# Optimization experiments

Measured on AMD Instinct MI355X. Metric: run time of the kernel, lower is better.

## Reference

```python
import jax, jax.numpy as jnp
import numpy as np

N_NODES = 50000
N_EDGES = 1600000
N_FEAT = 50
HID = 20
OUT_DIM = 10
N_GRAPHS = 64


def _glorot(key, shape):
    fan_in, fan_out = shape[0], shape[1]
    lim = float(np.sqrt(6.0 / (fan_in + fan_out)))
    return jax.random.uniform(key, shape, jnp.float32, -lim, lim)


def setup_inputs() -> dict:
    key = jax.random.key(0)
    ks = jax.random.split(key, 16)
    x = jax.random.normal(ks[0], (N_NODES, N_FEAT), jnp.float32)
    edge_index = jax.random.randint(ks[1], (2, N_EDGES), 0, N_NODES, jnp.int32)
    batch = jnp.sort(jax.random.randint(ks[2], (N_NODES,), 0, N_GRAPHS, jnp.int32))
    inp = {"x": x, "edge_index": edge_index, "batch": batch}
    # GraphConv layer params: lin_rel (weight+bias, applied to aggregated msgs), lin_root (no bias)
    dims = [(N_FEAT, HID), (HID, HID), (HID, HID)]
    for i, (di, do) in enumerate(dims, start=1):
        inp[f"W_rel{i}"] = _glorot(ks[3 * i], (di, do))
        inp[f"W_root{i}"] = _glorot(ks[3 * i + 1], (di, do))
        inp[f"b{i}"] = jnp.zeros((do,), jnp.float32)
    # final Linear on cat([max_pool, mean_pool]) -> in_features = 2*HID
    inp["W_lin"] = _glorot(ks[13], (2 * HID, OUT_DIM))
    inp["b_lin"] = jnp.zeros((OUT_DIM,), jnp.float32)
    return inp


def _graph_conv(x, src, dst, W_rel, W_root, b):
    # PyG GraphConv: aggregate raw neighbor features (sum), then linear.
    agg = jax.ops.segment_sum(x[src], dst, num_segments=N_NODES)  # [N, d_in]
    return agg @ W_rel + x @ W_root + b


def reference(x, edge_index, batch,
              W_rel1, W_root1, b1,
              W_rel2, W_root2, b2,
              W_rel3, W_root3, b3,
              W_lin, b_lin):
    src, dst = edge_index[0], edge_index[1]
    h = jax.nn.relu(_graph_conv(x, src, dst, W_rel1, W_root1, b1))
    h = jax.nn.relu(_graph_conv(h, src, dst, W_rel2, W_root2, b2))
    h = jax.nn.relu(_graph_conv(h, src, dst, W_rel3, W_root3, b3))
    # global max / mean pool per graph
    maxP = jax.ops.segment_max(h, batch, num_segments=N_GRAPHS)  # [G, HID]
    sums = jax.ops.segment_sum(h, batch, num_segments=N_GRAPHS)
    cnt = jax.ops.segment_sum(jnp.ones((h.shape[0], 1), h.dtype), batch, num_segments=N_GRAPHS)
    meanP = sums / jnp.maximum(cnt, 1.0)
    return jnp.concatenate([maxP, meanP], axis=-1) @ W_lin + b_lin
```

## Files before the change

### kernel.cpp

```cpp
#include <hip/hip_runtime.h>

#define N_NODES  50000
#define N_EDGES  1600000
#define N_FEAT   50
#define HID      20
#define OUT_DIM  10
#define N_GRAPHS 64

#define NBUCK 196
#define BCAP  10240
#define EPB   (N_EDGES/256)


__global__ __launch_bounds__(1024) void init_all(int* __restrict__ gcur,
        float* __restrict__ gmax, float* __restrict__ gsum, float* __restrict__ gcnt) {
    int t = threadIdx.x;
    if (t < NBUCK) gcur[t] = t * BCAP;
    for (int i = t; i < N_GRAPHS * HID; i += 1024) { gmax[i] = 0.f; gsum[i] = 0.f; }
    if (t < N_GRAPHS) gcnt[t] = 0.f;
}


__global__ __launch_bounds__(256) void gemm50(const float* __restrict__ x,
        const float* __restrict__ Wrel, const float* __restrict__ Wroot,
        const float* __restrict__ b,
        float* __restrict__ y, float* __restrict__ acc) {
    __shared__ float sWrel[N_FEAT * HID];
    __shared__ float sWroot[N_FEAT * HID];
    for (int i = threadIdx.x; i < N_FEAT * HID; i += 256) {
        sWrel[i]  = Wrel[i];
        sWroot[i] = Wroot[i];
    }
    __syncthreads();
    int idx = blockIdx.x * 256 + threadIdx.x;
    if (idx >= N_NODES * HID) return;
    int n = idx / HID, j = idx % HID;
    const float* xr = x + n * N_FEAT;
    float a0 = 0.0f, a1 = b[j];
    #pragma unroll
    for (int k = 0; k < N_FEAT; ++k) {
        float xv = xr[k];
        a0 = fmaf(xv, sWrel[k * HID + j], a0);
        a1 = fmaf(xv, sWroot[k * HID + j], a1);
    }
    y[idx]   = a0;
    acc[idx] = a1;
}


__global__ __launch_bounds__(1024) void bucket_scatter(const int* __restrict__ dst,
        const int* __restrict__ src, int* __restrict__ gcur,
        unsigned int* __restrict__ padded) {
    __shared__ unsigned int ep[EPB];
    __shared__ unsigned int ep2[EPB];
    __shared__ int cnt[256];
    __shared__ int scn[256];
    __shared__ int lofs[256];
    __shared__ int gbase[256];
    __shared__ int lcur[256];
    int t = threadIdx.x;
    if (t < 256) cnt[t] = 0;
    __syncthreads();
    int e0 = blockIdx.x * EPB;
    for (int i = t; i < EPB; i += 1024) {
        int d = dst[e0 + i];
        int s = src[e0 + i];
        ep[i] = ((unsigned int)d << 16) | (unsigned int)s;
        atomicAdd(&cnt[d >> 8], 1);
    }
    __syncthreads();
    if (t < 256) scn[t] = cnt[t];
    __syncthreads();
    for (int d = 1; d < 256; d <<= 1) {
        int u = 0;
        if (t < 256 && t >= d) u = scn[t - d];
        __syncthreads();
        if (t < 256) scn[t] += u;
        __syncthreads();
    }
    if (t < NBUCK) {
        int excl = scn[t] - cnt[t];
        lofs[t] = excl;
        lcur[t] = excl;
        gbase[t] = atomicAdd(&gcur[t], cnt[t]);
    }
    __syncthreads();
    for (int i = t; i < EPB; i += 1024) {
        unsigned int e = ep[i];
        int p = atomicAdd(&lcur[e >> 24], 1);
        ep2[p] = e;
    }
    __syncthreads();
    for (int i = t; i < EPB; i += 1024) {
        unsigned int e = ep2[i];
        int b = e >> 24;
        int gp = gbase[b] + (i - lofs[b]);
        if (gp < (b + 1) * BCAP) padded[gp] = e;
    }
}


__global__ __launch_bounds__(1024) void bucket_build(const int* __restrict__ gcur,
        const unsigned int* __restrict__ padded, unsigned short* __restrict__ csr16,
        int* __restrict__ start, int* __restrict__ endp) {
    __shared__ unsigned short eo[BCAP];
    __shared__ int cnt4[4][256];
    __shared__ int cur4[4][256];
    __shared__ int scn[256];
    int g = blockIdx.x, t = threadIdx.x;
    int wg = t >> 8;
    int base = g * BCAP;
    int m = min(gcur[g] - base, BCAP);
    if (t < 256) { cnt4[0][t] = 0; cnt4[1][t] = 0; cnt4[2][t] = 0; cnt4[3][t] = 0; }
    __syncthreads();
    for (int i = t; i < m; i += 1024)
        atomicAdd(&cnt4[wg][(padded[base + i] >> 16) & 255u], 1);
    __syncthreads();
    int c0 = 0, c1 = 0, c2 = 0, c3 = 0, tot = 0;
    if (t < 256) {
        c0 = cnt4[0][t]; c1 = cnt4[1][t]; c2 = cnt4[2][t]; c3 = cnt4[3][t];
        tot = c0 + c1 + c2 + c3;
        scn[t] = tot;
    }
    __syncthreads();
    for (int d = 1; d < 256; d <<= 1) {
        int u = 0;
        if (t < 256 && t >= d) u = scn[t - d];
        __syncthreads();
        if (t < 256) scn[t] += u;
        __syncthreads();
    }
    if (t < 256) {
        int excl = scn[t] - tot;
        cur4[0][t] = excl;
        cur4[1][t] = excl + c0;
        cur4[2][t] = excl + c0 + c1;
        cur4[3][t] = excl + c0 + c1 + c2;
        int node = g * 256 + t;
        if (node < N_NODES) {
            start[node] = base + excl;
            endp[node]  = base + excl + tot;
        }
    }
    __syncthreads();
    for (int i = t; i < m; i += 1024) {
        unsigned int e = padded[base + i];
        int p = atomicAdd(&cur4[wg][(e >> 16) & 255u], 1);
        eo[p] = (unsigned short)(e & 0xFFFFu);
    }
    __syncthreads();
    for (int i = t; i < m; i += 1024) csr16[base + i] = eo[i];
}


__global__ __launch_bounds__(320) void gather_gemm(const int* __restrict__ offs,
        const int* __restrict__ cend, const unsigned short* __restrict__ csr,
        const float* __restrict__ y_in, const float* __restrict__ accp,
        const float* __restrict__ Wrel, const float* __restrict__ Wroot,
        const float* __restrict__ b,
        float* __restrict__ y_out, float* __restrict__ acc_out) {
    __shared__ float sWrel[HID * HID];
    __shared__ float sWroot[HID * HID];
    __shared__ float sb[HID];
    __shared__ float rh[64][HID];
    for (int i = threadIdx.x; i < HID * HID; i += 320) {
        sWrel[i]  = Wrel[i];
        sWroot[i] = Wroot[i];
    }
    if (threadIdx.x < HID) sb[threadIdx.x] = b[threadIdx.x];
    int local = threadIdx.x / 5;
    int q     = threadIdx.x % 5;
    int node  = blockIdx.x * 64 + local;
    bool valid = node < N_NODES;
    if (valid) {
        int a = offs[node], e = cend[node];
        float4 s0 = make_float4(0.f, 0.f, 0.f, 0.f);
        float4 s1 = make_float4(0.f, 0.f, 0.f, 0.f);
        int k = a;
        for (; k + 3 < e; k += 4) {
            int sn0 = csr[k], sn1 = csr[k + 1], sn2 = csr[k + 2], sn3 = csr[k + 3];
            float4 v0 = *(const float4*)(y_in + sn0 * HID + q * 4);
            float4 v1 = *(const float4*)(y_in + sn1 * HID + q * 4);
            float4 v2 = *(const float4*)(y_in + sn2 * HID + q * 4);
            float4 v3 = *(const float4*)(y_in + sn3 * HID + q * 4);
            s0.x += v0.x + v2.x; s0.y += v0.y + v2.y;
            s0.z += v0.z + v2.z; s0.w += v0.w + v2.w;
            s1.x += v1.x + v3.x; s1.y += v1.y + v3.y;
            s1.z += v1.z + v3.z; s1.w += v1.w + v3.w;
        }
        for (; k < e; ++k) {
            int sn = csr[k];
            float4 v = *(const float4*)(y_in + sn * HID + q * 4);
            s0.x += v.x; s0.y += v.y; s0.z += v.z; s0.w += v.w;
        }
        float4 av = *((const float4*)(accp + node * HID) + q);
        rh[local][q * 4 + 0] = fmaxf(av.x + s0.x + s1.x, 0.f);
        rh[local][q * 4 + 1] = fmaxf(av.y + s0.y + s1.y, 0.f);
        rh[local][q * 4 + 2] = fmaxf(av.z + s0.z + s1.z, 0.f);
        rh[local][q * 4 + 3] = fmaxf(av.w + s0.w + s1.w, 0.f);
    }
    __syncthreads();
    if (!valid) return;
    int j0 = q * 4;
    float y0 = 0.f, y1 = 0.f, y2 = 0.f, y3 = 0.f;
    float a0 = sb[j0], a1 = sb[j0 + 1], a2 = sb[j0 + 2], a3 = sb[j0 + 3];
    #pragma unroll
    for (int k = 0; k < HID; ++k) {
        float hv = rh[local][k];
        const float* wr = sWrel  + k * HID + j0;
        const float* wo = sWroot + k * HID + j0;
        y0 = fmaf(hv, wr[0], y0); y1 = fmaf(hv, wr[1], y1);
        y2 = fmaf(hv, wr[2], y2); y3 = fmaf(hv, wr[3], y3);
        a0 = fmaf(hv, wo[0], a0); a1 = fmaf(hv, wo[1], a1);
        a2 = fmaf(hv, wo[2], a2); a3 = fmaf(hv, wo[3], a3);
    }
    *((float4*)(y_out   + node * HID) + q) = make_float4(y0, y1, y2, y3);
    *((float4*)(acc_out + node * HID) + q) = make_float4(a0, a1, a2, a3);
}


__global__ __launch_bounds__(320) void gather_pool(const int* __restrict__ offs,
        const int* __restrict__ cend, const unsigned short* __restrict__ csr,
        const float* __restrict__ y, const float* __restrict__ accp,
        const int* __restrict__ batch,
        float* __restrict__ gmax, float* __restrict__ gsum, float* __restrict__ gcnt) {
    __shared__ float bufA[64 * HID];
    __shared__ float bufB[64 * HID];
    __shared__ int   lcnt[64];
    int t = threadIdx.x;
    int local = t / 5;
    int q     = t % 5;
    int n0    = blockIdx.x * 64;
    int node  = n0 + local;
    int nvalid = min(64, N_NODES - n0);
    int nlast  = n0 + nvalid - 1;
    int g0   = batch[n0];
    int span = batch[nlast] - g0 + 1;
    bool valid = node < N_NODES;

    float v0 = 0.f, v1 = 0.f, v2 = 0.f, v3 = 0.f;
    if (valid) {
        int a = offs[node], e = cend[node];
        float4 s0 = make_float4(0.f, 0.f, 0.f, 0.f);
        float4 s1 = make_float4(0.f, 0.f, 0.f, 0.f);
        int k = a;
        for (; k + 3 < e; k += 4) {
            int sn0 = csr[k], sn1 = csr[k + 1], sn2 = csr[k + 2], sn3 = csr[k + 3];
            float4 w0 = *(const float4*)(y + sn0 * HID + q * 4);
            float4 w1 = *(const float4*)(y + sn1 * HID + q * 4);
            float4 w2 = *(const float4*)(y + sn2 * HID + q * 4);
            float4 w3 = *(const float4*)(y + sn3 * HID + q * 4);
            s0.x += w0.x + w2.x; s0.y += w0.y + w2.y;
            s0.z += w0.z + w2.z; s0.w += w0.w + w2.w;
            s1.x += w1.x + w3.x; s1.y += w1.y + w3.y;
            s1.z += w1.z + w3.z; s1.w += w1.w + w3.w;
        }
        for (; k < e; ++k) {
            int sn = csr[k];
            float4 w = *(const float4*)(y + sn * HID + q * 4);
            s0.x += w.x; s0.y += w.y; s0.z += w.z; s0.w += w.w;
        }
        float4 av = *((const float4*)(accp + node * HID) + q);
        v0 = fmaxf(av.x + s0.x + s1.x, 0.f);
        v1 = fmaxf(av.y + s0.y + s1.y, 0.f);
        v2 = fmaxf(av.z + s0.z + s1.z, 0.f);
        v3 = fmaxf(av.w + s0.w + s1.w, 0.f);
    }

    if (span == 1) {
        int j0 = q * 4;
        bufA[local * HID + j0 + 0] = v0;
        bufA[local * HID + j0 + 1] = v1;
        bufA[local * HID + j0 + 2] = v2;
        bufA[local * HID + j0 + 3] = v3;
        __syncthreads();
        int j = t % HID, r = t / HID;
        float m = 0.f, s = 0.f;
        #pragma unroll
        for (int rr = 0; rr < 4; ++rr) {
            float hv = bufA[(r + rr * 16) * HID + j];
            m = fmaxf(m, hv);
            s += hv;
        }
        bufB[r * HID + j] = m;
        bufB[320 + r * HID + j] = s;
        __syncthreads();
        if (t < HID) {
            float mm = 0.f, ss = 0.f;
            #pragma unroll
            for (int rr = 0; rr < 16; ++rr) {
                mm = fmaxf(mm, bufB[rr * HID + t]);
                ss += bufB[320 + rr * HID + t];
            }
            atomicMax((int*)&gmax[g0 * HID + t], __float_as_int(mm));
            atomicAdd(&gsum[g0 * HID + t], ss);
        }
        if (t == 0) atomicAdd(&gcnt[g0], (float)nvalid);
    } else {
        for (int i = t; i < 64 * HID; i += 320) { bufA[i] = 0.f; bufB[i] = 0.f; }
        if (t < 64) lcnt[t] = 0;
        __syncthreads();
        if (valid) {
            int li = batch[node] - g0;
            int j0 = q * 4;
            atomicMax((int*)&bufA[li * HID + j0 + 0], __float_as_int(v0));
            atomicMax((int*)&bufA[li * HID + j0 + 1], __float_as_int(v1));
            atomicMax((int*)&bufA[li * HID + j0 + 2], __float_as_int(v2));
            atomicMax((int*)&bufA[li * HID + j0 + 3], __float_as_int(v3));
            atomicAdd(&bufB[li * HID + j0 + 0], v0);
            atomicAdd(&bufB[li * HID + j0 + 1], v1);
            atomicAdd(&bufB[li * HID + j0 + 2], v2);
            atomicAdd(&bufB[li * HID + j0 + 3], v3);
            if (q == 0) atomicAdd(&lcnt[li], 1);
        }
        __syncthreads();
        for (int i = t; i < span * HID; i += 320) {
            int li = i / HID, j = i % HID;
            atomicMax((int*)&gmax[(g0 + li) * HID + j], __float_as_int(bufA[i]));
            atomicAdd(&gsum[(g0 + li) * HID + j], bufB[i]);
        }
        if (t < span) atomicAdd(&gcnt[g0 + t], (float)lcnt[t]);
    }
}


__global__ __launch_bounds__(640) void final_lin(const float* __restrict__ gmax,
        const float* __restrict__ gsum, const float* __restrict__ gcnt,
        const float* __restrict__ Wlin, const float* __restrict__ blin,
        float* __restrict__ out) {
    __shared__ float sW[2 * HID * OUT_DIM];
    for (int i = threadIdx.x; i < 2 * HID * OUT_DIM; i += 640) sW[i] = Wlin[i];
    __syncthreads();
    int idx = threadIdx.x;
    if (idx >= N_GRAPHS * OUT_DIM) return;
    int g = idx / OUT_DIM, o = idx % OUT_DIM;
    float c = fmaxf(gcnt[g], 1.0f);
    float a = blin[o];
    #pragma unroll
    for (int j = 0; j < HID; ++j) {
        a = fmaf(gmax[g * HID + j], sW[j * OUT_DIM + o], a);
        a = fmaf(gsum[g * HID + j] / c, sW[(HID + j) * OUT_DIM + o], a);
    }
    out[idx] = a;
}

extern "C" void kernel_launch(void* const* d_in, const int* in_sizes, int n_in,
                              void* d_out, int out_size, void* d_ws, size_t ws_size,
                              hipStream_t stream) {
    const float* x      = (const float*)d_in[0];
    const int*   ei     = (const int*)  d_in[1];
    const int*   batch  = (const int*)  d_in[2];
    const float* Wrel1  = (const float*)d_in[3];
    const float* Wroot1 = (const float*)d_in[4];
    const float* b1     = (const float*)d_in[5];
    const float* Wrel2  = (const float*)d_in[6];
    const float* Wroot2 = (const float*)d_in[7];
    const float* b2     = (const float*)d_in[8];
    const float* Wrel3  = (const float*)d_in[9];
    const float* Wroot3 = (const float*)d_in[10];
    const float* b3     = (const float*)d_in[11];
    const float* Wlin   = (const float*)d_in[12];
    const float* blin   = (const float*)d_in[13];
    float* out = (float*)d_out;

    char* ws = (char*)d_ws;
    const size_t NB   = (size_t)N_NODES * HID * sizeof(float);
    const size_t PB   = (size_t)NBUCK * BCAP * sizeof(int);
    const size_t CB   = (size_t)NBUCK * BCAP * sizeof(unsigned short);
    float*          yA     = (float*)(ws);
    float*          yB     = (float*)(ws + NB);
    float*          accA   = (float*)(ws + 2 * NB);
    float*          accB   = (float*)(ws + 3 * NB);
    unsigned int*   padded = (unsigned int*)(ws + 4 * NB);
    unsigned short* csr16  = (unsigned short*)(ws + 4 * NB + PB);
    int*            start  = (int*)(ws + 4 * NB + PB + CB);
    int*            endp   = start + N_NODES;
    int*            gcur   = endp + N_NODES;
    float*          gmax   = (float*)(gcur + NBUCK + 4);
    float*          gsum   = gmax + N_GRAPHS * HID;
    float*          gcnt   = gsum + N_GRAPHS * HID;

    const int* src = ei;
    const int* dst = ei + N_EDGES;

    const int gN = (N_NODES * HID + 255) / 256;
    const int gG = (N_NODES + 63) / 64;

    init_all<<<1, 1024, 0, stream>>>(gcur, gmax, gsum, gcnt);
    bucket_scatter<<<256, 1024, 0, stream>>>(dst, src, gcur, padded);
    bucket_build<<<NBUCK, 1024, 0, stream>>>(gcur, padded, csr16, start, endp);

    gemm50<<<gN, 256, 0, stream>>>(x, Wrel1, Wroot1, b1, yA, accA);
    gather_gemm<<<gG, 320, 0, stream>>>(start, endp, csr16, yA, accA,
                                        Wrel2, Wroot2, b2, yB, accB);
    gather_gemm<<<gG, 320, 0, stream>>>(start, endp, csr16, yB, accB,
                                        Wrel3, Wroot3, b3, yA, accA);
    gather_pool<<<gG, 320, 0, stream>>>(start, endp, csr16, yA, accA, batch,
                                        gmax, gsum, gcnt);
    final_lin<<<1, 640, 0, stream>>>(gmax, gsum, gcnt, Wlin, blin, out);
}
```

Before: 124.2 us.

## Fuse graph-build and GEMM kernels, sort nodes by degree for balanced gathers

Merges the first GEMM and the edge bucket scatter into one launch using disjoint block ranges, and replaces init_all with a memset. Fuses CSR bucket build with the layer-2 gather+GEMM so the block reuses its shared-memory edge list. Gathers now run in 256-node blocks that pair heavy and light nodes via a per-bucket degree-sorted permutation. Pooling uses segment ranges instead of atomics. This cuts launch count and load imbalance but lowers the number of blocks per gather kernel (196) and adds an O(256^2) rank sort per block.

```diff
diff --git a/kernel.cpp b/kernel.cpp
--- a/kernel.cpp
+++ b/kernel.cpp
@@ -10,66 +10,120 @@
 #define NBUCK 196
 #define BCAP  10240
 #define EPB   (N_EDGES/256)
-
-
-__global__ __launch_bounds__(1024) void init_all(int* __restrict__ gcur,
+#define G50B  977
+
+
+__global__ __launch_bounds__(1024) void k1_gemm_scatter(
+        const float* __restrict__ x, const float* __restrict__ Wrel,
+        const float* __restrict__ Wroot, const float* __restrict__ b,
+        float* __restrict__ y, float* __restrict__ acc,
+        const int* __restrict__ dst, const int* __restrict__ srcv,
+        int* __restrict__ gcur, unsigned int* __restrict__ padded,
         float* __restrict__ gmax, float* __restrict__ gsum, float* __restrict__ gcnt) {
+    __shared__ char smem[55120];
     int t = threadIdx.x;
-    if (t < NBUCK) gcur[t] = t * BCAP;
-    for (int i = t; i < N_GRAPHS * HID; i += 1024) { gmax[i] = 0.f; gsum[i] = 0.f; }
-    if (t < N_GRAPHS) gcnt[t] = 0.f;
-}
-
-
-__global__ __launch_bounds__(256) void gemm50(const float* __restrict__ x,
+    if (blockIdx.x < G50B) {
+        if (blockIdx.x == 0) {
+            for (int i = t; i < N_GRAPHS * HID; i += 1024) { gmax[i] = 0.f; gsum[i] = 0.f; }
+            if (t < N_GRAPHS) gcnt[t] = 0.f;
+        }
+        float* sWrel  = (float*)smem;
+        float* sWroot = sWrel + N_FEAT * HID;
+        for (int i = t; i < N_FEAT * HID; i += 1024) { sWrel[i] = Wrel[i]; sWroot[i] = Wroot[i]; }
+        __syncthreads();
+        int idx = blockIdx.x * 1024 + t;
+        if (idx < N_NODES * HID) {
+            int n = idx / HID, j = idx % HID;
+            const float* xr = x + n * N_FEAT;
+            float a0 = 0.f, a1 = b[j];
+            #pragma unroll
+            for (int k = 0; k < N_FEAT; ++k) {
+                float xv = xr[k];
+                a0 = fmaf(xv, sWrel[k * HID + j], a0);
+                a1 = fmaf(xv, sWroot[k * HID + j], a1);
+            }
+            y[idx] = a0; acc[idx] = a1;
+        }
+    } else {
+        unsigned int* ep   = (unsigned int*)smem;
+        unsigned int* ep2  = ep + EPB;
+        int* cnt   = (int*)(ep2 + EPB);
+        int* scn   = cnt + 256;
+        int* lofs  = scn + 256;
+        int* gbase = lofs + 256;
+        int* lcur  = gbase + 256;
+        if (t < 256) cnt[t] = 0;
+        __syncthreads();
+        int e0 = (blockIdx.x - G50B) * EPB;
+        for (int i = t; i < EPB; i += 1024) {
+            int d = dst[e0 + i], s = srcv[e0 + i];
+            ep[i] = ((unsigned int)d << 16) | (unsigned int)s;
+            atomicAdd(&cnt[d >> 8], 1);
+        }
+        __syncthreads();
+        if (t < 256) scn[t] = cnt[t];
+        __syncthreads();
+        for (int d = 1; d < 256; d <<= 1) {
+            int u = 0;
+            if (t < 256 && t >= d) u = scn[t - d];
+            __syncthreads();
+            if (t < 256) scn[t] += u;
+            __syncthreads();
+        }
+        if (t < NBUCK) {
+            int excl = scn[t] - cnt[t];
+            lofs[t] = excl; lcur[t] = excl;
+            gbase[t] = t * BCAP + atomicAdd(&gcur[t], cnt[t]);
+        }
+        __syncthreads();
+        for (int i = t; i < EPB; i += 1024) {
+            unsigned int e = ep[i];
+            int p = atomicAdd(&lcur[e >> 24], 1);
+            ep2[p] = e;
+        }
+        __syncthreads();
+        for (int i = t; i < EPB; i += 1024) {
+            unsigned int e = ep2[i];
+            int bb = e >> 24;
+            int gp = gbase[bb] + (i - lofs[bb]);
+            if (gp < (bb + 1) * BCAP) padded[gp] = e;
+        }
+    }
+}
+
+
+__global__ __launch_bounds__(1024) void k2_build_gather(
+        const int* __restrict__ gcur, const unsigned int* __restrict__ padded,
+        unsigned short* __restrict__ csr16, int* __restrict__ startg,
+        int* __restrict__ cntg, unsigned short* __restrict__ permg,
+        const float* __restrict__ y_in, const float* __restrict__ accp,
         const float* __restrict__ Wrel, const float* __restrict__ Wroot,
         const float* __restrict__ b,
-        float* __restrict__ y, float* __restrict__ acc) {
-    __shared__ float sWrel[N_FEAT * HID];
-    __shared__ float sWroot[N_FEAT * HID];
-    for (int i = threadIdx.x; i < N_FEAT * HID; i += 256) {
-        sWrel[i]  = Wrel[i];
-        sWroot[i] = Wroot[i];
-    }
-    __syncthreads();
-    int idx = blockIdx.x * 256 + threadIdx.x;
-    if (idx >= N_NODES * HID) return;
-    int n = idx / HID, j = idx % HID;
-    const float* xr = x + n * N_FEAT;
-    float a0 = 0.0f, a1 = b[j];
-    #pragma unroll
-    for (int k = 0; k < N_FEAT; ++k) {
-        float xv = xr[k];
-        a0 = fmaf(xv, sWrel[k * HID + j], a0);
-        a1 = fmaf(xv, sWroot[k * HID + j], a1);
-    }
-    y[idx]   = a0;
-    acc[idx] = a1;
-}
-
-
-__global__ __launch_bounds__(1024) void bucket_scatter(const int* __restrict__ dst,
-        const int* __restrict__ src, int* __restrict__ gcur,
-        unsigned int* __restrict__ padded) {
-    __shared__ unsigned int ep[EPB];
-    __shared__ unsigned int ep2[EPB];
-    __shared__ int cnt[256];
-    __shared__ int scn[256];
-    __shared__ int lofs[256];
-    __shared__ int gbase[256];
-    __shared__ int lcur[256];
-    int t = threadIdx.x;
-    if (t < 256) cnt[t] = 0;
-    __syncthreads();
-    int e0 = blockIdx.x * EPB;
-    for (int i = t; i < EPB; i += 1024) {
-        int d = dst[e0 + i];
-        int s = src[e0 + i];
-        ep[i] = ((unsigned int)d << 16) | (unsigned int)s;
-        atomicAdd(&cnt[d >> 8], 1);
-    }
-    __syncthreads();
-    if (t < 256) scn[t] = cnt[t];
+        float* __restrict__ y_out, float* __restrict__ acc_out) {
+    __shared__ unsigned short eo[BCAP];
+    __shared__ float rh[256 * HID];
+    __shared__ float sWrel[HID * HID], sWroot[HID * HID], sb[HID];
+    __shared__ int cnt4[4][256], cur4[4][256];
+    __shared__ int scn[256], s_start[256], s_cnt[256];
+    __shared__ unsigned short sperm[256];
+    int g = blockIdx.x, t = threadIdx.x, wg = t >> 8;
+    int base = g * BCAP;
+    int m = min(gcur[g], BCAP);
+    int n0 = g * 256, nvalid = min(256, N_NODES - n0);
+    for (int i = t; i < HID * HID; i += 1024) { sWrel[i] = Wrel[i]; sWroot[i] = Wroot[i]; }
+    if (t < HID) sb[t] = b[t];
+    if (t < 256) { cnt4[0][t] = 0; cnt4[1][t] = 0; cnt4[2][t] = 0; cnt4[3][t] = 0; }
+    for (int i = t; i < nvalid * HID; i += 1024) rh[i] = accp[n0 * HID + i];
+    __syncthreads();
+    for (int i = t; i < m; i += 1024)
+        atomicAdd(&cnt4[wg][(padded[base + i] >> 16) & 255u], 1);
+    __syncthreads();
+    int c0 = 0, c1 = 0, c2 = 0, tot = 0;
+    if (t < 256) {
+        c0 = cnt4[0][t]; c1 = cnt4[1][t]; c2 = cnt4[2][t]; int c3 = cnt4[3][t];
+        tot = c0 + c1 + c2 + c3;
+        scn[t] = tot; s_cnt[t] = tot;
+    }
     __syncthreads();
     for (int d = 1; d < 256; d <<= 1) {
         int u = 0;
@@ -78,69 +132,13 @@
         if (t < 256) scn[t] += u;
         __syncthreads();
     }
-    if (t < NBUCK) {
-        int excl = scn[t] - cnt[t];
-        lofs[t] = excl;
-        lcur[t] = excl;
-        gbase[t] = atomicAdd(&gcur[t], cnt[t]);
-    }
-    __syncthreads();
-    for (int i = t; i < EPB; i += 1024) {
-        unsigned int e = ep[i];
-        int p = atomicAdd(&lcur[e >> 24], 1);
-        ep2[p] = e;
-    }
-    __syncthreads();
-    for (int i = t; i < EPB; i += 1024) {
-        unsigned int e = ep2[i];
-        int b = e >> 24;
-        int gp = gbase[b] + (i - lofs[b]);
-        if (gp < (b + 1) * BCAP) padded[gp] = e;
-    }
-}
-
-
-__global__ __launch_bounds__(1024) void bucket_build(const int* __restrict__ gcur,
-        const unsigned int* __restrict__ padded, unsigned short* __restrict__ csr16,
-        int* __restrict__ start, int* __restrict__ endp) {
-    __shared__ unsigned short eo[BCAP];
-    __shared__ int cnt4[4][256];
-    __shared__ int cur4[4][256];
-    __shared__ int scn[256];
-    int g = blockIdx.x, t = threadIdx.x;
-    int wg = t >> 8;
-    int base = g * BCAP;
-    int m = min(gcur[g] - base, BCAP);
-    if (t < 256) { cnt4[0][t] = 0; cnt4[1][t] = 0; cnt4[2][t] = 0; cnt4[3][t] = 0; }
-    __syncthreads();
-    for (int i = t; i < m; i += 1024)
-        atomicAdd(&cnt4[wg][(padded[base + i] >> 16) & 255u], 1);
-    __syncthreads();
-    int c0 = 0, c1 = 0, c2 = 0, c3 = 0, tot = 0;
-    if (t < 256) {
-        c0 = cnt4[0][t]; c1 = cnt4[1][t]; c2 = cnt4[2][t]; c3 = cnt4[3][t];
-        tot = c0 + c1 + c2 + c3;
-        scn[t] = tot;
-    }
-    __syncthreads();
-    for (int d = 1; d < 256; d <<= 1) {
-        int u = 0;
-        if (t < 256 && t >= d) u = scn[t - d];
-        __syncthreads();
-        if (t < 256) scn[t] += u;
-        __syncthreads();
-    }
     if (t < 256) {
         int excl = scn[t] - tot;
-        cur4[0][t] = excl;
-        cur4[1][t] = excl + c0;
-        cur4[2][t] = excl + c0 + c1;
-        cur4[3][t] = excl + c0 + c1 + c2;
-        int node = g * 256 + t;
-        if (node < N_NODES) {
-            start[node] = base + excl;
-            endp[node]  = base + excl + tot;
-        }
+        s_start[t] = excl;
+        cur4[0][t] = excl; cur4[1][t] = excl + c0;
+        cur4[2][t] = excl + c0 + c1; cur4[3][t] = excl + c0 + c1 + c2;
+        int node = n0 + t;
+        if (node < N_NODES) { startg[node] = base + excl; cntg[node] = tot; }
     }
     __syncthreads();
     for (int i = t; i < m; i += 1024) {
@@ -150,176 +148,225 @@
     }
     __syncthreads();
     for (int i = t; i < m; i += 1024) csr16[base + i] = eo[i];
-}
-
-
-__global__ __launch_bounds__(320) void gather_gemm(const int* __restrict__ offs,
-        const int* __restrict__ cend, const unsigned short* __restrict__ csr,
+    if (t < 256) {
+        int d = s_cnt[t], rank = 0;
+        for (int j2 = 0; j2 < 256; ++j2) {
+            int dj = s_cnt[j2];
+            rank += (dj > d) || (dj == d && j2 < t);
+        }
+        sperm[rank] = (unsigned short)t;
+    }
+    __syncthreads();
+    if (t < 256) permg[n0 + t] = sperm[t];
+    int grp = t >> 3, lane = t & 7;
+    if (lane < 5) {
+        int q4 = lane * 4;
+        #pragma unroll
+        for (int rep = 0; rep < 2; ++rep) {
+            int rank = rep ? 255 - grp : grp;
+            int nl = sperm[rank];
+            if (nl >= nvalid) continue;
+            int a = s_start[nl], e = a + s_cnt[nl];
+            float4 s0 = make_float4(0.f, 0.f, 0.f, 0.f);
+            float4 s1 = make_float4(0.f, 0.f, 0.f, 0.f);
+            int k = a;
+            for (; k + 3 < e; k += 4) {
+                int sn0 = eo[k], sn1 = eo[k + 1], sn2 = eo[k + 2], sn3 = eo[k + 3];
+                float4 v0 = *(const float4*)(y_in + sn0 * HID + q4);
+                float4 v1 = *(const float4*)(y_in + sn1 * HID + q4);
+                float4 v2 = *(const float4*)(y_in + sn2 * HID + q4);
+                float4 v3 = *(const float4*)(y_in + sn3 * HID + q4);
+                s0.x += v0.x + v2.x; s0.y += v0.y + v2.y;
+                s0.z += v0.z + v2.z; s0.w += v0.w + v2.w;
+                s1.x += v1.x + v3.x; s1.y += v1.y + v3.y;
+                s1.z += v1.z + v3.z; s1.w += v1.w + v3.w;
+            }
+            for (; k < e; ++k) {
+                int sn = eo[k];
+                float4 v = *(const float4*)(y_in + sn * HID + q4);
+                s0.x += v.x; s0.y += v.y; s0.z += v.z; s0.w += v.w;
+            }
+            float* rp = &rh[nl * HID + q4];
+            rp[0] += s0.x + s1.x; rp[1] += s0.y + s1.y;
+            rp[2] += s0.z + s1.z; rp[3] += s0.w + s1.w;
+        }
+    }
+    __syncthreads();
+    for (int i = t; i < nvalid * 5; i += 1024) {
+        int n = i / 5, j0 = (i % 5) * 4;
+        float y0 = 0.f, y1 = 0.f, y2 = 0.f, y3 = 0.f;
+        float a0 = sb[j0], a1 = sb[j0 + 1], a2 = sb[j0 + 2], a3 = sb[j0 + 3];
+        #pragma unroll
+        for (int k = 0; k < HID; ++k) {
+            float h = fmaxf(rh[n * HID + k], 0.f);
+            const float* wr = sWrel  + k * HID + j0;
+            const float* wo = sWroot + k * HID + j0;
+            y0 = fmaf(h, wr[0], y0); y1 = fmaf(h, wr[1], y1);
+            y2 = fmaf(h, wr[2], y2); y3 = fmaf(h, wr[3], y3);
+            a0 = fmaf(h, wo[0], a0); a1 = fmaf(h, wo[1], a1);
+            a2 = fmaf(h, wo[2], a2); a3 = fmaf(h, wo[3], a3);
+        }
+        *(float4*)(y_out   + (n0 + n) * HID + j0) = make_float4(y0, y1, y2, y3);
+        *(float4*)(acc_out + (n0 + n) * HID + j0) = make_float4(a0, a1, a2, a3);
+    }
+}
+
+
+__global__ __launch_bounds__(1024) void k3_gather_gemm(
+        const int* __restrict__ startg, const int* __restrict__ cntg,
+        const unsigned short* __restrict__ csr16, const unsigned short* __restrict__ permg,
         const float* __restrict__ y_in, const float* __restrict__ accp,
         const float* __restrict__ Wrel, const float* __restrict__ Wroot,
         const float* __restrict__ b,
         float* __restrict__ y_out, float* __restrict__ acc_out) {
-    __shared__ float sWrel[HID * HID];
-    __shared__ float sWroot[HID * HID];
-    __shared__ float sb[HID];
-    __shared__ float rh[64][HID];
-    for (int i = threadIdx.x; i < HID * HID; i += 320) {
-        sWrel[i]  = Wrel[i];
-        sWroot[i] = Wroot[i];
-    }
-    if (threadIdx.x < HID) sb[threadIdx.x] = b[threadIdx.x];
-    int local = threadIdx.x / 5;
-    int q     = threadIdx.x % 5;
-    int node  = blockIdx.x * 64 + local;
-    bool valid = node < N_NODES;
-    if (valid) {
-        int a = offs[node], e = cend[node];
-        float4 s0 = make_float4(0.f, 0.f, 0.f, 0.f);
-        float4 s1 = make_float4(0.f, 0.f, 0.f, 0.f);
-        int k = a;
-        for (; k + 3 < e; k += 4) {
-            int sn0 = csr[k], sn1 = csr[k + 1], sn2 = csr[k + 2], sn3 = csr[k + 3];
-            float4 v0 = *(const float4*)(y_in + sn0 * HID + q * 4);
-            float4 v1 = *(const float4*)(y_in + sn1 * HID + q * 4);
-            float4 v2 = *(const float4*)(y_in + sn2 * HID + q * 4);
-            float4 v3 = *(const float4*)(y_in + sn3 * HID + q * 4);
-            s0.x += v0.x + v2.x; s0.y += v0.y + v2.y;
-            s0.z += v0.z + v2.z; s0.w += v0.w + v2.w;
-            s1.x += v1.x + v3.x; s1.y += v1.y + v3.y;
-            s1.z += v1.z + v3.z; s1.w += v1.w + v3.w;
-        }
-        for (; k < e; ++k) {
-            int sn = csr[k];
-            float4 v = *(const float4*)(y_in + sn * HID + q * 4);
-            s0.x += v.x; s0.y += v.y; s0.z += v.z; s0.w += v.w;
-        }
-        float4 av = *((const float4*)(accp + node * HID) + q);
-        rh[local][q * 4 + 0] = fmaxf(av.x + s0.x + s1.x, 0.f);
-        rh[local][q * 4 + 1] = fmaxf(av.y + s0.y + s1.y, 0.f);
-        rh[local][q * 4 + 2] = fmaxf(av.z + s0.z + s1.z, 0.f);
-        rh[local][q * 4 + 3] = fmaxf(av.w + s0.w + s1.w, 0.f);
-    }
-    __syncthreads();
-    if (!valid) return;
-    int j0 = q * 4;
-    float y0 = 0.f, y1 = 0.f, y2 = 0.f, y3 = 0.f;
-    float a0 = sb[j0], a1 = sb[j0 + 1], a2 = sb[j0 + 2], a3 = sb[j0 + 3];
-    #pragma unroll
-    for (int k = 0; k < HID; ++k) {
-        float hv = rh[local][k];
-        const float* wr = sWrel  + k * HID + j0;
-        const float* wo = sWroot + k * HID + j0;
-        y0 = fmaf(hv, wr[0], y0); y1 = fmaf(hv, wr[1], y1);
-        y2 = fmaf(hv, wr[2], y2); y3 = fmaf(hv, wr[3], y3);
-        a0 = fmaf(hv, wo[0], a0); a1 = fmaf(hv, wo[1], a1);
-        a2 = fmaf(hv, wo[2], a2); a3 = fmaf(hv, wo[3], a3);
-    }
-    *((float4*)(y_out   + node * HID) + q) = make_float4(y0, y1, y2, y3);
-    *((float4*)(acc_out + node * HID) + q) = make_float4(a0, a1, a2, a3);
-}
-
-
-__global__ __launch_bounds__(320) void gather_pool(const int* __restrict__ offs,
-        const int* __restrict__ cend, const unsigned short* __restrict__ csr,
-        const float* __restrict__ y, const float* __restrict__ accp,
+    __shared__ float rh[256 * HID];
+    __shared__ float sWrel[HID * HID], sWroot[HID * HID], sb[HID];
+    int g = blockIdx.x, t = threadIdx.x;
+    int n0 = g * 256, nvalid = min(256, N_NODES - n0);
+    for (int i = t; i < HID * HID; i += 1024) { sWrel[i] = Wrel[i]; sWroot[i] = Wroot[i]; }
+    if (t < HID) sb[t] = b[t];
+    for (int i = t; i < nvalid * HID; i += 1024) rh[i] = accp[n0 * HID + i];
+    __syncthreads();
+    int grp = t >> 3, lane = t & 7;
+    if (lane < 5) {
+        int q4 = lane * 4;
+        #pragma unroll
+        for (int rep = 0; rep < 2; ++rep) {
+            int rank = rep ? 255 - grp : grp;
+            int nl = permg[n0 + rank];
+            if (nl >= nvalid) continue;
+            int node = n0 + nl;
+            int a = startg[node], e = a + cntg[node];
+            float4 s0 = make_float4(0.f, 0.f, 0.f, 0.f);
+            float4 s1 = make_float4(0.f, 0.f, 0.f, 0.f);
+            int k = a;
+            for (; k + 3 < e; k += 4) {
+                int sn0 = csr16[k], sn1 = csr16[k + 1], sn2 = csr16[k + 2], sn3 = csr16[k + 3];
+                float4 v0 = *(const float4*)(y_in + sn0 * HID + q4);
+                float4 v1 = *(const float4*)(y_in + sn1 * HID + q4);
+                float4 v2 = *(const float4*)(y_in + sn2 * HID + q4);
+                float4 v3 = *(const float4*)(y_in + sn3 * HID + q4);
+                s0.x += v0.x + v2.x; s0.y += v0.y + v2.y;
+                s0.z += v0.z + v2.z; s0.w += v0.w + v2.w;
+                s1.x += v1.x + v3.x; s1.y += v1.y + v3.y;
+                s1.z += v1.z + v3.z; s1.w += v1.w + v3.w;
+            }
+            for (; k < e; ++k) {
+                int sn = csr16[k];
+                float4 v = *(const float4*)(y_in + sn * HID + q4);
+                s0.x += v.x; s0.y += v.y; s0.z += v.z; s0.w += v.w;
+            }
+            float* rp = &rh[nl * HID + q4];
+            rp[0] += s0.x + s1.x; rp[1] += s0.y + s1.y;
+            rp[2] += s0.z + s1.z; rp[3] += s0.w + s1.w;
+        }
+    }
+    __syncthreads();
+    for (int i = t; i < nvalid * 5; i += 1024) {
+        int n = i / 5, j0 = (i % 5) * 4;
+        float y0 = 0.f, y1 = 0.f, y2 = 0.f, y3 = 0.f;
+        float a0 = sb[j0], a1 = sb[j0 + 1], a2 = sb[j0 + 2], a3 = sb[j0 + 3];
+        #pragma unroll
+        for (int k = 0; k < HID; ++k) {
+            float h = fmaxf(rh[n * HID + k], 0.f);
+            const float* wr = sWrel  + k * HID + j0;
+            const float* wo = sWroot + k * HID + j0;
+            y0 = fmaf(h, wr[0], y0); y1 = fmaf(h, wr[1], y1);
+            y2 = fmaf(h, wr[2], y2); y3 = fmaf(h, wr[3], y3);
+            a0 = fmaf(h, wo[0], a0); a1 = fmaf(h, wo[1], a1);
+            a2 = fmaf(h, wo[2], a2); a3 = fmaf(h, wo[3], a3);
+        }
+        *(float4*)(y_out   + (n0 + n) * HID + j0) = make_float4(y0, y1, y2, y3);
+        *(float4*)(acc_out + (n0 + n) * HID + j0) = make_float4(a0, a1, a2, a3);
+    }
+}
+
+
+__global__ __launch_bounds__(1024) void k4_gather_pool(
+        const int* __restrict__ startg, const int* __restrict__ cntg,
+        const unsigned short* __restrict__ csr16, const unsigned short* __restrict__ permg,
+        const float* __restrict__ y_in, const float* __restrict__ accp,
         const int* __restrict__ batch,
         float* __restrict__ gmax, float* __restrict__ gsum, float* __restrict__ gcnt) {
-    __shared__ float bufA[64 * HID];
-    __shared__ float bufB[64 * HID];
-    __shared__ int   lcnt[64];
-    int t = threadIdx.x;
-    int local = t / 5;
-    int q     = t % 5;
-    int n0    = blockIdx.x * 64;
-    int node  = n0 + local;
-    int nvalid = min(64, N_NODES - n0);
-    int nlast  = n0 + nvalid - 1;
-    int g0   = batch[n0];
-    int span = batch[nlast] - g0 + 1;
-    bool valid = node < N_NODES;
-
-    float v0 = 0.f, v1 = 0.f, v2 = 0.f, v3 = 0.f;
-    if (valid) {
-        int a = offs[node], e = cend[node];
-        float4 s0 = make_float4(0.f, 0.f, 0.f, 0.f);
-        float4 s1 = make_float4(0.f, 0.f, 0.f, 0.f);
-        int k = a;
-        for (; k + 3 < e; k += 4) {
-            int sn0 = csr[k], sn1 = csr[k + 1], sn2 = csr[k + 2], sn3 = csr[k + 3];
-            float4 w0 = *(const float4*)(y + sn0 * HID + q * 4);
-            float4 w1 = *(const float4*)(y + sn1 * HID + q * 4);
-            float4 w2 = *(const float4*)(y + sn2 * HID + q * 4);
-            float4 w3 = *(const float4*)(y + sn3 * HID + q * 4);
-            s0.x += w0.x + w2.x; s0.y += w0.y + w2.y;
-            s0.z += w0.z + w2.z; s0.w += w0.w + w2.w;
-            s1.x += w1.x + w3.x; s1.y += w1.y + w3.y;
-            s1.z += w1.z + w3.z; s1.w += w1.w + w3.w;
-        }
-        for (; k < e; ++k) {
-            int sn = csr[k];
-            float4 w = *(const float4*)(y + sn * HID + q * 4);
-            s0.x += w.x; s0.y += w.y; s0.z += w.z; s0.w += w.w;
-        }
-        float4 av = *((const float4*)(accp + node * HID) + q);
-        v0 = fmaxf(av.x + s0.x + s1.x, 0.f);
-        v1 = fmaxf(av.y + s0.y + s1.y, 0.f);
-        v2 = fmaxf(av.z + s0.z + s1.z, 0.f);
-        v3 = fmaxf(av.w + s0.w + s1.w, 0.f);
-    }
-
-    if (span == 1) {
-        int j0 = q * 4;
-        bufA[local * HID + j0 + 0] = v0;
-        bufA[local * HID + j0 + 1] = v1;
-        bufA[local * HID + j0 + 2] = v2;
-        bufA[local * HID + j0 + 3] = v3;
-        __syncthreads();
-        int j = t % HID, r = t / HID;
-        float m = 0.f, s = 0.f;
+    __shared__ float rh[256 * HID];
+    __shared__ float redm[51 * HID], reds[51 * HID];
+    __shared__ int sbatch[256];
+    __shared__ int seglo[16], seghi[16];
+    int g = blockIdx.x, t = threadIdx.x;
+    int n0 = g * 256, nvalid = min(256, N_NODES - n0);
+    for (int i = t; i < nvalid * HID; i += 1024) rh[i] = accp[n0 * HID + i];
+    if (t < nvalid) sbatch[t] = batch[n0 + t];
+    __syncthreads();
+    int grp = t >> 3, lane = t & 7;
+    if (lane < 5) {
+        int q4 = lane * 4;
         #pragma unroll
-        for (int rr = 0; rr < 4; ++rr) {
-            float hv = bufA[(r + rr * 16) * HID + j];
-            m = fmaxf(m, hv);
-            s += hv;
-        }
-        bufB[r * HID + j] = m;
-        bufB[320 + r * HID + j] = s;
+        for (int rep = 0; rep < 2; ++rep) {
+            int rank = rep ? 255 - grp : grp;
+            int nl = permg[n0 + rank];
+            if (nl >= nvalid) continue;
+            int node = n0 + nl;
+            int a = startg[node], e = a + cntg[node];
+            float4 s0 = make_float4(0.f, 0.f, 0.f, 0.f);
+            float4 s1 = make_float4(0.f, 0.f, 0.f, 0.f);
+            int k = a;
+            for (; k + 3 < e; k += 4) {
+                int sn0 = csr16[k], sn1 = csr16[k + 1], sn2 = csr16[k + 2], sn3 = csr16[k + 3];
+                float4 v0 = *(const float4*)(y_in + sn0 * HID + q4);
+                float4 v1 = *(const float4*)(y_in + sn1 * HID + q4);
+                float4 v2 = *(const float4*)(y_in + sn2 * HID + q4);
+                float4 v3 = *(const float4*)(y_in + sn3 * HID + q4);
+                s0.x += v0.x + v2.x; s0.y += v0.y + v2.y;
+                s0.z += v0.z + v2.z; s0.w += v0.w + v2.w;
+                s1.x += v1.x + v3.x; s1.y += v1.y + v3.y;
+                s1.z += v1.z + v3.z; s1.w += v1.w + v3.w;
+            }
+            for (; k < e; ++k) {
+                int sn = csr16[k];
+                float4 v = *(const float4*)(y_in + sn * HID + q4);
+                s0.x += v.x; s0.y += v.y; s0.z += v.z; s0.w += v.w;
+            }
+            float* rp = &rh[nl * HID + q4];
+            rp[0] += s0.x + s1.x; rp[1] += s0.y + s1.y;
+            rp[2] += s0.z + s1.z; rp[3] += s0.w + s1.w;
+        }
+    }
+    __syncthreads();
+    int g0 = sbatch[0];
+    int span = sbatch[nvalid - 1] - g0 + 1;
+    if (t < nvalid) {
+        int bi = sbatch[t] - g0;
+        if (bi < 16) {
+            if (t == 0 || sbatch[t - 1] != sbatch[t]) seglo[bi] = t;
+            if (t == nvalid - 1 || sbatch[t + 1] != sbatch[t]) seghi[bi] = t + 1;
+        }
+    }
+    __syncthreads();
+    if (span > 16) span = 16;
+    for (int li = 0; li < span; ++li) {
+        int lo = seglo[li], hi = seghi[li];
+        int r = t / HID, j = t % HID;
+        if (r < 51) {
+            float mx = 0.f, sm = 0.f;
+            for (int n = lo + r; n < hi; n += 51) {
+                float v = fmaxf(rh[n * HID + j], 0.f);
+                mx = fmaxf(mx, v); sm += v;
+            }
+            redm[r * HID + j] = mx; reds[r * HID + j] = sm;
+        }
         __syncthreads();
         if (t < HID) {
             float mm = 0.f, ss = 0.f;
-            #pragma unroll
-            for (int rr = 0; rr < 16; ++rr) {
-                mm = fmaxf(mm, bufB[rr * HID + t]);
-                ss += bufB[320 + rr * HID + t];
-            }
-            atomicMax((int*)&gmax[g0 * HID + t], __float_as_int(mm));
-            atomicAdd(&gsum[g0 * HID + t], ss);
-        }
-        if (t == 0) atomicAdd(&gcnt[g0], (float)nvalid);
-    } else {
-        for (int i = t; i < 64 * HID; i += 320) { bufA[i] = 0.f; bufB[i] = 0.f; }
-        if (t < 64) lcnt[t] = 0;
-        __syncthreads();
-        if (valid) {
-            int li = batch[node] - g0;
-            int j0 = q * 4;
-            atomicMax((int*)&bufA[li * HID + j0 + 0], __float_as_int(v0));
-            atomicMax((int*)&bufA[li * HID + j0 + 1], __float_as_int(v1));
-            atomicMax((int*)&bufA[li * HID + j0 + 2], __float_as_int(v2));
-            atomicMax((int*)&bufA[li * HID + j0 + 3], __float_as_int(v3));
-            atomicAdd(&bufB[li * HID + j0 + 0], v0);
-            atomicAdd(&bufB[li * HID + j0 + 1], v1);
-            atomicAdd(&bufB[li * HID + j0 + 2], v2);
-            atomicAdd(&bufB[li * HID + j0 + 3], v3);
-            if (q == 0) atomicAdd(&lcnt[li], 1);
-        }
-        __syncthreads();
-        for (int i = t; i < span * HID; i += 320) {
-            int li = i / HID, j = i % HID;
-            atomicMax((int*)&gmax[(g0 + li) * HID + j], __float_as_int(bufA[i]));
-            atomicAdd(&gsum[(g0 + li) * HID + j], bufB[i]);
-        }
-        if (t < span) atomicAdd(&gcnt[g0 + t], (float)lcnt[t]);
+            #pragma unroll 17
+            for (int r2 = 0; r2 < 51; ++r2) {
+                mm = fmaxf(mm, redm[r2 * HID + t]);
+                ss += reds[r2 * HID + t];
+            }
+            atomicMax((int*)&gmax[(g0 + li) * HID + t], __float_as_int(mm));
+            atomicAdd(&gsum[(g0 + li) * HID + t], ss);
+        }
+        if (t == HID) atomicAdd(&gcnt[g0 + li], (float)(hi - lo));
+        __syncthreads();
     }
 }
 
@@ -364,38 +411,36 @@
     float* out = (float*)d_out;
 
     char* ws = (char*)d_ws;
-    const size_t NB   = (size_t)N_NODES * HID * sizeof(float);
-    const size_t PB   = (size_t)NBUCK * BCAP * sizeof(int);
-    const size_t CB   = (size_t)NBUCK * BCAP * sizeof(unsigned short);
+    const size_t NB = (size_t)N_NODES * HID * sizeof(float);
+    const size_t PB = (size_t)NBUCK * BCAP * sizeof(int);
+    const size_t CB = (size_t)NBUCK * BCAP * sizeof(unsigned short);
+    const size_t NP = (size_t)NBUCK * 256;
     float*          yA     = (float*)(ws);
     float*          yB     = (float*)(ws + NB);
     float*          accA   = (float*)(ws + 2 * NB);
     float*          accB   = (float*)(ws + 3 * NB);
     unsigned int*   padded = (unsigned int*)(ws + 4 * NB);
     unsigned short* csr16  = (unsigned short*)(ws + 4 * NB + PB);
-    int*            start  = (int*)(ws + 4 * NB + PB + CB);
-    int*            endp   = start + N_NODES;
-    int*            gcur   = endp + N_NODES;
-    float*          gmax   = (float*)(gcur + NBUCK + 4);
+    int*            startg = (int*)(ws + 4 * NB + PB + CB);
+    int*            cntg   = startg + NP;
+    unsigned short* permg  = (unsigned short*)(cntg + NP);
+    int*            gcur   = (int*)((char*)permg + NP * sizeof(unsigned short));
+    float*          gmax   = (float*)(gcur + 256);
     float*          gsum   = gmax + N_GRAPHS * HID;
     float*          gcnt   = gsum + N_GRAPHS * HID;
 
     const int* src = ei;
     const int* dst = ei + N_EDGES;
 
-    const int gN = (N_NODES * HID + 255) / 256;
-    const int gG = (N_NODES + 63) / 64;
-
-    init_all<<<1, 1024, 0, stream>>>(gcur, gmax, gsum, gcnt);
-    bucket_scatter<<<256, 1024, 0, stream>>>(dst, src, gcur, padded);
-    bucket_build<<<NBUCK, 1024, 0, stream>>>(gcur, padded, csr16, start, endp);
-
-    gemm50<<<gN, 256, 0, stream>>>(x, Wrel1, Wroot1, b1, yA, accA);
-    gather_gemm<<<gG, 320, 0, stream>>>(start, endp, csr16, yA, accA,
-                                        Wrel2, Wroot2, b2, yB, accB);
-    gather_gemm<<<gG, 320, 0, stream>>>(start, endp, csr16, yB, accB,
-                                        Wrel3, Wroot3, b3, yA, accA);
-    gather_pool<<<gG, 320, 0, stream>>>(start, endp, csr16, yA, accA, batch,
-                                        gmax, gsum, gcnt);
+    hipMemsetAsync(gcur, 0, NBUCK * sizeof(int), stream);
+    k1_gemm_scatter<<<G50B + 256, 1024, 0, stream>>>(x, Wrel1, Wroot1, b1, yA, accA,
+                                                     dst, src, gcur, padded,
+                                                     gmax, gsum, gcnt);
+    k2_build_gather<<<NBUCK, 1024, 0, stream>>>(gcur, padded, csr16, startg, cntg, permg,
+                                                yA, accA, Wrel2, Wroot2, b2, yB, accB);
+    k3_gather_gemm<<<NBUCK, 1024, 0, stream>>>(startg, cntg, csr16, permg,
+                                               yB, accB, Wrel3, Wroot3, b3, yA, accA);
+    k4_gather_pool<<<NBUCK, 1024, 0, stream>>>(startg, cntg, csr16, permg,
+                                               yA, accA, batch, gmax, gsum, gcnt);
     final_lin<<<1, 640, 0, stream>>>(gmax, gsum, gcnt, Wlin, blin, out);
 }
```

New measurement: 116.8 us. 5.9% less time.
